# Optimization experiments

Hardware: AMD Instinct MI355X
Metric: run time of the kernel (lower is better)

Reference implementation:

```python
import jax, jax.numpy as jnp
import numpy as np

GROUPS = 32
EPS = 1e-5

def setup_inputs() -> dict:
    key = jax.random.key(0)
    ks = jax.random.split(key, 3)
    b, c, h, w = 4, 256, 64, 64
    x = jax.random.normal(ks[0], (b, c, h, w), dtype=jnp.float32)
    gn_w = jnp.ones((c,), jnp.float32)
    gn_b = jnp.zeros((c,), jnp.float32)
    qkv_w = jax.random.normal(ks[1], (3 * c, c), jnp.float32) * (1.0 / np.sqrt(c))
    qkv_b = jnp.zeros((3 * c,), jnp.float32)
    out_w = jax.random.normal(ks[2], (c, c), jnp.float32) * (1.0 / np.sqrt(c))
    out_b = jnp.zeros((c,), jnp.float32)
    return {"x": x, "gn_w": gn_w, "gn_b": gn_b, "qkv_w": qkv_w,
            "qkv_b": qkv_b, "out_w": out_w, "out_b": out_b}

def reference(x, gn_w, gn_b, qkv_w, qkv_b, out_w, out_b):
    b, c, h, w = x.shape
    scale = c ** (-0.5)
    # GroupNorm over (c/groups, h, w) per group, per-channel affine
    xg = x.reshape(b, GROUPS, c // GROUPS, h, w)
    mean = xg.mean(axis=(2, 3, 4), keepdims=True)
    var = xg.var(axis=(2, 3, 4), keepdims=True)
    xn = ((xg - mean) * jax.lax.rsqrt(var + EPS)).reshape(b, c, h, w)
    xn = xn * gn_w[None, :, None, None] + gn_b[None, :, None, None]
    # 1x1 conv to qkv: [b,3c,h,w]
    qkv = jnp.einsum('bchw,oc->bohw', xn, qkv_w) + qkv_b[None, :, None, None]
    q, k, v = jnp.split(qkv, 3, axis=1)
    # hw_to_seq: [b,c,h,w] -> [b, n, c]
    to_seq = lambda t: t.reshape(b, c, h * w).transpose(0, 2, 1)
    q, k, v = to_seq(q), to_seq(k), to_seq(v)
    sim = jnp.einsum('bic,bjc->bij', q, k) * scale  # [b,n,n]
    attn = jax.nn.softmax(sim, axis=-1)
    out = jnp.einsum('bij,bjc->bic', attn, v)  # [b,n,c]
    out = out.transpose(0, 2, 1).reshape(b, c, h, w)
    out = jnp.einsum('bchw,oc->bohw', out, out_w) + out_b[None, :, None, None]
    return out + x
```

## Files before the change

kernel.cpp:

```cpp
#include <hip/hip_runtime.h>
#include <hip/hip_bf16.h>
#include <stdint.h>

typedef __attribute__((ext_vector_type(8))) short bf16x8;
typedef __attribute__((ext_vector_type(4))) float f32x4;
typedef __attribute__((ext_vector_type(16))) float f32x16;

typedef __attribute__((address_space(1))) const uint32_t gu32;
typedef __attribute__((address_space(3))) uint32_t lu32;

#define N_PIX 4096
#define C_CH  256
#define KVB   128
#define SCALE_LOG2E (0.0625f * 1.4426950408889634f)

__device__ __forceinline__ unsigned short f2bf(float f) {
    unsigned int u = __float_as_uint(f);
    unsigned int r = (u + 0x7FFFu + ((u >> 16) & 1u)) >> 16;
    return (unsigned short)r;
}
__device__ __forceinline__ float bf2f(short s) {
    return __uint_as_float(((unsigned int)(unsigned short)s) << 16);
}

__global__ void prep_kernel(const float* __restrict__ x,
                            const float* __restrict__ gn_w,
                            const float* __restrict__ gn_b,
                            const float* __restrict__ qkv_w,
                            const float* __restrict__ out_w,
                            float* __restrict__ a_out,
                            float* __restrict__ b_out,
                            unsigned short* __restrict__ wq,
                            unsigned short* __restrict__ w2) {
    int bid = blockIdx.x;
    if (bid >= 128) {
        int i = (bid - 128) * 256 + threadIdx.x;
        wq[i] = f2bf(qkv_w[i]);
        if (i < 65536) w2[i] = f2bf(out_w[i]);
        return;
    }
    int b = bid >> 5, g = bid & 31;
    const float* base = x + ((size_t)(b * C_CH + g * 8)) * N_PIX;
    float s1 = 0.f, s2 = 0.f;
    for (int i = threadIdx.x; i < 8 * N_PIX; i += 256) {
        float v = base[i];
        s1 += v; s2 += v * v;
    }
    __shared__ float r1[256], r2[256];
    r1[threadIdx.x] = s1; r2[threadIdx.x] = s2;
    __syncthreads();
    for (int off = 128; off > 0; off >>= 1) {
        if (threadIdx.x < off) {
            r1[threadIdx.x] += r1[threadIdx.x + off];
            r2[threadIdx.x] += r2[threadIdx.x + off];
        }
        __syncthreads();
    }
    if (threadIdx.x < 8) {
        float mean = r1[0] * (1.f / 32768.f);
        float var  = r2[0] * (1.f / 32768.f) - mean * mean;
        float rstd = rsqrtf(var + 1e-5f);
        int c = g * 8 + threadIdx.x;
        float A = rstd * gn_w[c];
        a_out[b * C_CH + c] = A;
        b_out[b * C_CH + c] = gn_b[c] - mean * A;
    }
}

__global__ __launch_bounds__(256)
void qkv_gemm_kernel(const float* __restrict__ x,
                     const float* __restrict__ a_arr,
                     const float* __restrict__ bb_arr,
                     const unsigned short* __restrict__ wq,
                     const float* __restrict__ qkv_b,
                     unsigned short* __restrict__ q_seq,
                     unsigned short* __restrict__ k_seq,
                     unsigned short* __restrict__ vT) {
    __shared__ char wlds[2][16384];
    int pb   = blockIdx.x;
    int och  = blockIdx.y;
    int b    = blockIdx.z;
    int tid  = threadIdx.x;
    int wave = tid >> 6;
    int lane = tid & 63;
    int lo = lane & 15, hi = lane >> 4;
    int prow = pb * 64 + wave * 16 + lo;
    const float* xb = x + (size_t)b * C_CH * N_PIX;
    const float* av = a_arr + b * C_CH;
    const float* bv = bb_arr + b * C_CH;

    auto stageW = [&](int buf, int ks) {
#pragma unroll
        for (int pass = 0; pass < 4; pass++) {
            int chunk = pass * 256 + tid;
            int r = chunk >> 2, cslot = chunk & 3;
            const char* src = (const char*)wq + (size_t)(och * 256 + r) * 512
                              + ks * 64 + cslot * 16;
            __builtin_amdgcn_global_load_lds((gu32*)src,
                                             (lu32*)(wlds[buf] + chunk * 16), 16, 0, 0);
        }
    };

    f32x4 acc[16];
#pragma unroll
    for (int t = 0; t < 16; t++) acc[t] = (f32x4)0.f;

    stageW(0, 0);
    __syncthreads();

#pragma unroll
    for (int ks = 0; ks < 8; ks++) {
        int buf = ks & 1;
        if (ks < 7) stageW(buf ^ 1, ks + 1);
        int c0 = ks * 32 + hi * 8;
        bf16x8 afrag;
#pragma unroll
        for (int i = 0; i < 8; i++) {
            float xv = xb[(size_t)(c0 + i) * N_PIX + prow];
            float v  = fmaf(av[c0 + i], xv, bv[c0 + i]);
            afrag[i] = (short)f2bf(v);
        }
#pragma unroll
        for (int t = 0; t < 16; t++) {
            bf16x8 bfrag = *(const bf16x8*)(wlds[buf] + (t * 16 + lo) * 64 + hi * 16);
            acc[t] = __builtin_amdgcn_mfma_f32_16x16x32_bf16(afrag, bfrag, acc[t], 0, 0, 0);
        }
        __syncthreads();
    }

    int p_base = pb * 64 + wave * 16 + hi * 4;
#pragma unroll
    for (int t = 0; t < 16; t++) {
        int o = och * 256 + t * 16 + lo;
        float bias = qkv_b[o];
        if (och == 2) {
            ushort4 pk;
            pk.x = f2bf(acc[t][0] + bias);
            pk.y = f2bf(acc[t][1] + bias);
            pk.z = f2bf(acc[t][2] + bias);
            pk.w = f2bf(acc[t][3] + bias);
            *(ushort4*)(vT + ((size_t)(b * C_CH + (o - 512))) * N_PIX + p_base) = pk;
        } else {
            float sc = (och == 0) ? SCALE_LOG2E : 1.f;
            unsigned short* dst = (och == 0 ? q_seq : k_seq) + (size_t)b * N_PIX * C_CH;
            int cc = o - och * 256;
#pragma unroll
            for (int r = 0; r < 4; r++)
                dst[(size_t)(p_base + r) * 256 + cc] = f2bf((acc[t][r] + bias) * sc);
        }
    }
}

__global__ __launch_bounds__(512, 2)
void attn_kernel(const unsigned short* __restrict__ q_seq,
                 const unsigned short* __restrict__ k_seq,
                 const unsigned short* __restrict__ vT,
                 unsigned short* __restrict__ o_part,
                 float* __restrict__ m_part,
                 float* __restrict__ l_part) {
    extern __shared__ char lds[];
    char* Kt = lds;
    char* Vt = lds + 65536;
    float* Ml = (float*)(lds + 131072);
    float* Ll = (float*)(lds + 132096);

    int bid  = blockIdx.x;
    int work = (bid & 7) * 32 + (bid >> 3);
    int group = work >> 5;
    int b    = group >> 1;
    int half = group & 1;
    int pq   = work & 31;
    int tid = threadIdx.x;
    int wave = tid >> 6, lane = tid & 63;
    int l31 = lane & 31, hi2 = lane >> 5;
    int qg = wave >> 1, kvh = wave & 1;
    int p0 = pq * 128 + qg * 32;

    const unsigned short* qb = q_seq + (size_t)b * N_PIX * C_CH;
    const unsigned short* kb = k_seq + (size_t)b * N_PIX * C_CH;
    const unsigned short* vb = vT    + (size_t)b * C_CH * N_PIX;

    int ktrow = tid >> 5, kcol = tid & 31;
    int vtrow = tid >> 4, vcol = tid & 15;

    bf16x8 qf[16];
#pragma unroll
    for (int cs = 0; cs < 16; cs++)
        qf[cs] = *(const bf16x8*)(qb + (size_t)(p0 + l31) * 256 + cs * 16 + hi2 * 8);

    f32x16 oacc[8];
#pragma unroll
    for (int t = 0; t < 8; t++) oacc[t] = (f32x16)0.f;
    float m = -1e30f, lsum = 0.f;

    int kswz = l31 << 4;
    int vswz = (l31 & 15) << 4;

    for (int t = 0; t < 16; t++) {
        if (t) __syncthreads();
        int j0 = half * 2048 + t * KVB;
#pragma unroll
        for (int p = 0; p < 8; p++) {
            int kr = p * 16 + ktrow;
            const char* ksrc = (const char*)(kb + (size_t)(j0 + kr) * 256)
                               + ((kcol ^ (kr & 31)) << 4);
            __builtin_amdgcn_global_load_lds((gu32*)ksrc, (lu32*)(Kt + p * 8192 + tid * 16), 16, 0, 0);
            int vr = p * 32 + vtrow;
            const char* vsrc = (const char*)(vb + (size_t)vr * N_PIX + j0)
                               + ((vcol ^ (vr & 15)) << 4);
            __builtin_amdgcn_global_load_lds((gu32*)vsrc, (lu32*)(Vt + p * 8192 + tid * 16), 16, 0, 0);
        }
        __syncthreads();

#pragma unroll
        for (int sub = 0; sub < 2; sub++) {
            int kvb = kvh * 64 + sub * 32;

            f32x16 sacc = (f32x16)0.f;
            __builtin_amdgcn_s_setprio(1);
#pragma unroll
            for (int cs = 0; cs < 16; cs++) {
                bf16x8 kf = *(const bf16x8*)(Kt + (kvb + l31) * 512 + ((cs * 32 + hi2 * 16) ^ kswz));
                sacc = __builtin_amdgcn_mfma_f32_32x32x16_bf16(kf, qf[cs], sacc, 0, 0, 0);
            }
            __builtin_amdgcn_s_setprio(0);

            float mx = sacc[0];
#pragma unroll
            for (int r = 1; r < 16; r++) mx = fmaxf(mx, sacc[r]);
            mx = fmaxf(mx, __shfl_xor(mx, 32, 64));
            if (__any(mx > m + 8.f)) {
                float mC = fmaxf(m, mx);
                float al = __builtin_amdgcn_exp2f(m - mC);
                m = mC; lsum *= al;
#pragma unroll
                for (int r = 0; r < 16; r++) {
                    int qr = (r & 3) + 8 * (r >> 2) + 4 * hi2;
                    float ar = __shfl(al, qr, 64);
#pragma unroll
                    for (int ct = 0; ct < 8; ct++) oacc[ct][r] *= ar;
                }
            }
            f32x16 pexp;
            float psum = 0.f;
#pragma unroll
            for (int r = 0; r < 16; r++) {
                float pe = __builtin_amdgcn_exp2f(sacc[r] - m);
                pexp[r] = pe; psum += pe;
            }
            psum += __shfl_xor(psum, 32, 64);
            lsum += psum;

            bf16x8 pa0, pa1;
            {
                unsigned int x0, x1, y0, y1;
                asm("v_cvt_pk_bf16_f32 %0, %1, %2" : "=v"(x0) : "v"(pexp[0]), "v"(pexp[1]));
                asm("v_cvt_pk_bf16_f32 %0, %1, %2" : "=v"(x1) : "v"(pexp[2]), "v"(pexp[3]));
                asm("v_cvt_pk_bf16_f32 %0, %1, %2" : "=v"(y0) : "v"(pexp[4]), "v"(pexp[5]));
                asm("v_cvt_pk_bf16_f32 %0, %1, %2" : "=v"(y1) : "v"(pexp[6]), "v"(pexp[7]));
                asm("v_permlane32_swap_b32 %0, %1" : "+v"(x0), "+v"(y0));
                asm("v_permlane32_swap_b32 %0, %1" : "+v"(x1), "+v"(y1));
                union { unsigned int u[4]; bf16x8 v; } f0;
                f0.u[0] = x0; f0.u[1] = x1; f0.u[2] = y0; f0.u[3] = y1;
                pa0 = f0.v;
                asm("v_cvt_pk_bf16_f32 %0, %1, %2" : "=v"(x0) : "v"(pexp[8]), "v"(pexp[9]));
                asm("v_cvt_pk_bf16_f32 %0, %1, %2" : "=v"(x1) : "v"(pexp[10]), "v"(pexp[11]));
                asm("v_cvt_pk_bf16_f32 %0, %1, %2" : "=v"(y0) : "v"(pexp[12]), "v"(pexp[13]));
                asm("v_cvt_pk_bf16_f32 %0, %1, %2" : "=v"(y1) : "v"(pexp[14]), "v"(pexp[15]));
                asm("v_permlane32_swap_b32 %0, %1" : "+v"(x0), "+v"(y0));
                asm("v_permlane32_swap_b32 %0, %1" : "+v"(x1), "+v"(y1));
                union { unsigned int u[4]; bf16x8 v; } f1;
                f1.u[0] = x0; f1.u[1] = x1; f1.u[2] = y0; f1.u[3] = y1;
                pa1 = f1.v;
            }

            __builtin_amdgcn_s_setprio(1);
#pragma unroll
            for (int ct = 0; ct < 8; ct++) {
                int c = ct * 32 + l31;
                bf16x8 vf0 = *(const bf16x8*)(Vt + c * 256 + ((kvb * 2 + hi2 * 16) ^ vswz));
                oacc[ct] = __builtin_amdgcn_mfma_f32_32x32x16_bf16(pa0, vf0, oacc[ct], 0, 0, 0);
                bf16x8 vf1 = *(const bf16x8*)(Vt + c * 256 + ((kvb * 2 + 32 + hi2 * 16) ^ vswz));
                oacc[ct] = __builtin_amdgcn_mfma_f32_32x32x16_bf16(pa1, vf1, oacc[ct], 0, 0, 0);
            }
            __builtin_amdgcn_s_setprio(0);
        }
    }
    __syncthreads();

    char* Ow = lds + wave * 16384;
#pragma unroll
    for (int ct = 0; ct < 8; ct++) {
#pragma unroll
        for (int r = 0; r < 16; r++) {
            int q = (r & 3) + 8 * (r >> 2) + 4 * hi2;
            int cb = (ct * 32 + l31) * 2;
            *(unsigned short*)(Ow + q * 512 + (cb ^ (q << 4))) = f2bf(oacc[ct][r]);
        }
    }
    if (lane < 32) { Ml[wave * 32 + lane] = m; Ll[wave * 32 + lane] = lsum; }
    __syncthreads();

    int ql = tid >> 2;
    int qr = ql & 31, qg2 = ql >> 5;
    float g[2];
    float m0 = Ml[(qg2 * 2 + 0) * 32 + qr];
    float m1 = Ml[(qg2 * 2 + 1) * 32 + qr];
    float mm = fmaxf(m0, m1);
    g[0] = __builtin_amdgcn_exp2f(m0 - mm);
    g[1] = __builtin_amdgcn_exp2f(m1 - mm);
    float ls = g[0] * Ll[(qg2 * 2 + 0) * 32 + qr] + g[1] * Ll[(qg2 * 2 + 1) * 32 + qr];
    int qglob = pq * 128 + ql;
    size_t pbase = (size_t)(half * 4 + b) * N_PIX;
    if ((tid & 3) == 0) {
        m_part[pbase + qglob] = mm;
        l_part[pbase + qglob] = ls;
    }
    unsigned short* orow = o_part + (pbase + qglob) * C_CH;
#pragma unroll
    for (int i = 0; i < 8; i++) {
        int s = i * 4 + (tid & 3);
        int cb = (s * 16) ^ (qr << 4);
        bf16x8 a0 = *(const bf16x8*)(lds + (size_t)(qg2 * 2 + 0) * 16384 + qr * 512 + cb);
        bf16x8 a1 = *(const bf16x8*)(lds + (size_t)(qg2 * 2 + 1) * 16384 + qr * 512 + cb);
        union { unsigned short u[8]; bf16x8 v; } pk;
#pragma unroll
        for (int j = 0; j < 8; j++)
            pk.u[j] = f2bf(g[0] * bf2f(a0[j]) + g[1] * bf2f(a1[j]));
        *(bf16x8*)(orow + s * 8) = pk.v;
    }
}

__global__ __launch_bounds__(256)
void combine_kernel(const unsigned short* __restrict__ o_part,
                    const float* __restrict__ m_part,
                    const float* __restrict__ l_part,
                    const unsigned short* __restrict__ w2,
                    const float* __restrict__ out_b,
                    const float* __restrict__ x,
                    float* __restrict__ y) {
    int bid = blockIdx.x;
    int b = bid >> 7, pr = bid & 127;
    int tid = threadIdx.x;
    int wave = tid >> 6, lane = tid & 63;
    int lo = lane & 15, hi = lane >> 4;
    int rowgrp = wave & 1, ohalf = wave >> 1;
    int p0 = pr * 32 + rowgrp * 16;
    int row = p0 + lo;
    size_t i0 = (size_t)b * N_PIX + row;
    size_t i1 = (size_t)(4 + b) * N_PIX + row;
    float m0 = m_part[i0], l0 = l_part[i0];
    float m1 = m_part[i1], l1 = l_part[i1];
    float mm = fmaxf(m0, m1);
    float e0 = __builtin_amdgcn_exp2f(m0 - mm), e1 = __builtin_amdgcn_exp2f(m1 - mm);
    float rl = 1.f / (l0 * e0 + l1 * e1);
    float f0 = e0 * rl, f1 = e1 * rl;
    const unsigned short* P0 = o_part + i0 * C_CH;
    const unsigned short* P1 = o_part + i1 * C_CH;

    f32x4 acc2[8];
#pragma unroll
    for (int t = 0; t < 8; t++) acc2[t] = (f32x4)0.f;

#pragma unroll
    for (int ks = 0; ks < 8; ks++) {
        int c0 = ks * 32 + hi * 8;
        bf16x8 a0 = *(const bf16x8*)(P0 + c0);
        bf16x8 a1 = *(const bf16x8*)(P1 + c0);
        bf16x8 of;
#pragma unroll
        for (int i = 0; i < 8; i++)
            of[i] = (short)f2bf(bf2f(a0[i]) * f0 + bf2f(a1[i]) * f1);
#pragma unroll
        for (int ot = 0; ot < 8; ot++) {
            int o = ohalf * 128 + ot * 16 + lo;
            bf16x8 wf = *(const bf16x8*)(w2 + (size_t)o * 256 + c0);
            acc2[ot] = __builtin_amdgcn_mfma_f32_16x16x32_bf16(of, wf, acc2[ot], 0, 0, 0);
        }
    }

    int p_base = p0 + hi * 4;
#pragma unroll
    for (int ot = 0; ot < 8; ot++) {
        int o = ohalf * 128 + ot * 16 + lo;
        float bias = out_b[o];
        size_t off = ((size_t)(b * C_CH + o)) * N_PIX + p_base;
        f32x4 xv = *(const f32x4*)(x + off);
        f32x4 outv;
#pragma unroll
        for (int r = 0; r < 4; r++) outv[r] = acc2[ot][r] + bias + xv[r];
        *(f32x4*)(y + off) = outv;
    }
}

extern "C" void kernel_launch(void* const* d_in, const int* in_sizes, int n_in,
                              void* d_out, int out_size, void* d_ws, size_t ws_size,
                              hipStream_t stream) {
    const float* x     = (const float*)d_in[0];
    const float* gn_w  = (const float*)d_in[1];
    const float* gn_b  = (const float*)d_in[2];
    const float* qkv_w = (const float*)d_in[3];
    const float* qkv_b = (const float*)d_in[4];
    const float* out_w = (const float*)d_in[5];
    const float* out_b = (const float*)d_in[6];
    float* y = (float*)d_out;
    char* ws = (char*)d_ws;

    float* a_arr  = (float*)(ws);
    float* bb_arr = (float*)(ws + 4096);
    unsigned short* wq     = (unsigned short*)(ws + 8192);
    unsigned short* w2     = (unsigned short*)(ws + 401408);
    unsigned short* q_seq  = (unsigned short*)(ws + 532480);
    unsigned short* k_seq  = (unsigned short*)(ws + 532480 + 8388608);
    unsigned short* vT     = (unsigned short*)(ws + 532480 + 2 * 8388608);
    unsigned short* o_part = (unsigned short*)(ws + 532480 + 3 * 8388608);
    float* m_part = (float*)(ws + 42475520);
    float* l_part = (float*)(ws + 42606592);

    (void)hipFuncSetAttribute((const void*)attn_kernel,
                              hipFuncAttributeMaxDynamicSharedMemorySize, 133120);

    prep_kernel<<<896, 256, 0, stream>>>(x, gn_w, gn_b, qkv_w, out_w,
                                         a_arr, bb_arr, wq, w2);
    qkv_gemm_kernel<<<dim3(64, 3, 4), 256, 0, stream>>>(x, a_arr, bb_arr, wq, qkv_b,
                                                        q_seq, k_seq, vT);
    attn_kernel<<<256, 512, 133120, stream>>>(q_seq, k_seq, vT, o_part, m_part, l_part);
    combine_kernel<<<512, 256, 0, stream>>>(o_part, m_part, l_part, w2, out_b, x, y);
}
```

Baseline: 173.2 us.

## Stage normalized activation tile in LDS once and loop over q/k/v outputs

The QKV GEMM now normalizes and converts a 64-pixel by 256-channel activation tile to bf16 once per block into a swizzled LDS buffer. It reuses that tile for all three output groups (q, k, v) instead of launching a separate block per group that each re-read x from global memory. This cuts redundant global reads and GroupNorm math by a factor of three. The cost is a third as many blocks (256 instead of 768), more dynamic LDS per block, and a longer serial loop per block, which may reduce parallelism.

```diff
diff --git a/kernel.cpp b/kernel.cpp
--- a/kernel.cpp
+++ b/kernel.cpp
@@ -76,20 +76,39 @@
                      unsigned short* __restrict__ q_seq,
                      unsigned short* __restrict__ k_seq,
                      unsigned short* __restrict__ vT) {
-    __shared__ char wlds[2][16384];
-    int pb   = blockIdx.x;
-    int och  = blockIdx.y;
-    int b    = blockIdx.z;
-    int tid  = threadIdx.x;
-    int wave = tid >> 6;
-    int lane = tid & 63;
+    extern __shared__ char qlds[];
+    char* Ab = qlds;
+    char* wlds0 = qlds + 32768;
+    char* wlds1 = qlds + 49152;
+    int pb = blockIdx.x;
+    int b  = blockIdx.y;
+    int tid = threadIdx.x;
+    int wave = tid >> 6, lane = tid & 63;
     int lo = lane & 15, hi = lane >> 4;
-    int prow = pb * 64 + wave * 16 + lo;
     const float* xb = x + (size_t)b * C_CH * N_PIX;
     const float* av = a_arr + b * C_CH;
     const float* bv = bb_arr + b * C_CH;
 
-    auto stageW = [&](int buf, int ks) {
+    {
+        int px = lane;
+        int cblk = wave;
+        int gpx = pb * 64 + px;
+#pragma unroll
+        for (int i = 0; i < 8; i++) {
+            int c0 = cblk * 64 + i * 8;
+            union { unsigned short u[8]; bf16x8 v; } pk;
+#pragma unroll
+            for (int j = 0; j < 8; j++) {
+                float xv = xb[(size_t)(c0 + j) * N_PIX + gpx];
+                pk.u[j] = f2bf(fmaf(av[c0 + j], xv, bv[c0 + j]));
+            }
+            int slot = ((c0 >> 3) ^ (px & 31));
+            *(bf16x8*)(Ab + px * 512 + slot * 16) = pk.v;
+        }
+    }
+
+    auto stageW = [&](char* dst, int w) {
+        int och = w >> 3, ks = w & 7;
 #pragma unroll
         for (int pass = 0; pass < 4; pass++) {
             int chunk = pass * 256 + tid;
@@ -97,56 +116,53 @@
             const char* src = (const char*)wq + (size_t)(och * 256 + r) * 512
                               + ks * 64 + cslot * 16;
             __builtin_amdgcn_global_load_lds((gu32*)src,
-                                             (lu32*)(wlds[buf] + chunk * 16), 16, 0, 0);
+                                             (lu32*)(dst + chunk * 16), 16, 0, 0);
         }
     };
 
-    f32x4 acc[16];
-#pragma unroll
-    for (int t = 0; t < 16; t++) acc[t] = (f32x4)0.f;
-
-    stageW(0, 0);
+    stageW(wlds0, 0);
     __syncthreads();
 
-#pragma unroll
-    for (int ks = 0; ks < 8; ks++) {
-        int buf = ks & 1;
-        if (ks < 7) stageW(buf ^ 1, ks + 1);
-        int c0 = ks * 32 + hi * 8;
-        bf16x8 afrag;
-#pragma unroll
-        for (int i = 0; i < 8; i++) {
-            float xv = xb[(size_t)(c0 + i) * N_PIX + prow];
-            float v  = fmaf(av[c0 + i], xv, bv[c0 + i]);
-            afrag[i] = (short)f2bf(v);
+    int p_base = pb * 64 + wave * 16 + hi * 4;
+    int arow = wave * 16 + lo;
+    for (int och = 0; och < 3; och++) {
+        f32x4 acc[16];
+#pragma unroll
+        for (int t = 0; t < 16; t++) acc[t] = (f32x4)0.f;
+#pragma unroll
+        for (int ks = 0; ks < 8; ks++) {
+            int w = och * 8 + ks;
+            char* cur = (w & 1) ? wlds1 : wlds0;
+            char* nxt = (w & 1) ? wlds0 : wlds1;
+            if (w < 23) stageW(nxt, w + 1);
+            int slot = (ks * 4 + hi) ^ (arow & 31);
+            bf16x8 afrag = *(const bf16x8*)(Ab + arow * 512 + slot * 16);
+#pragma unroll
+            for (int t = 0; t < 16; t++) {
+                bf16x8 bfrag = *(const bf16x8*)(cur + (t * 16 + lo) * 64 + hi * 16);
+                acc[t] = __builtin_amdgcn_mfma_f32_16x16x32_bf16(afrag, bfrag, acc[t], 0, 0, 0);
+            }
+            __syncthreads();
         }
 #pragma unroll
         for (int t = 0; t < 16; t++) {
-            bf16x8 bfrag = *(const bf16x8*)(wlds[buf] + (t * 16 + lo) * 64 + hi * 16);
-            acc[t] = __builtin_amdgcn_mfma_f32_16x16x32_bf16(afrag, bfrag, acc[t], 0, 0, 0);
-        }
-        __syncthreads();
-    }
-
-    int p_base = pb * 64 + wave * 16 + hi * 4;
-#pragma unroll
-    for (int t = 0; t < 16; t++) {
-        int o = och * 256 + t * 16 + lo;
-        float bias = qkv_b[o];
-        if (och == 2) {
-            ushort4 pk;
-            pk.x = f2bf(acc[t][0] + bias);
-            pk.y = f2bf(acc[t][1] + bias);
-            pk.z = f2bf(acc[t][2] + bias);
-            pk.w = f2bf(acc[t][3] + bias);
-            *(ushort4*)(vT + ((size_t)(b * C_CH + (o - 512))) * N_PIX + p_base) = pk;
-        } else {
-            float sc = (och == 0) ? SCALE_LOG2E : 1.f;
-            unsigned short* dst = (och == 0 ? q_seq : k_seq) + (size_t)b * N_PIX * C_CH;
-            int cc = o - och * 256;
-#pragma unroll
-            for (int r = 0; r < 4; r++)
-                dst[(size_t)(p_base + r) * 256 + cc] = f2bf((acc[t][r] + bias) * sc);
+            int o = och * 256 + t * 16 + lo;
+            float bias = qkv_b[o];
+            if (och == 2) {
+                ushort4 pk;
+                pk.x = f2bf(acc[t][0] + bias);
+                pk.y = f2bf(acc[t][1] + bias);
+                pk.z = f2bf(acc[t][2] + bias);
+                pk.w = f2bf(acc[t][3] + bias);
+                *(ushort4*)(vT + ((size_t)(b * C_CH + (o - 512))) * N_PIX + p_base) = pk;
+            } else {
+                float sc = (och == 0) ? SCALE_LOG2E : 1.f;
+                unsigned short* dst = (och == 0 ? q_seq : k_seq) + (size_t)b * N_PIX * C_CH;
+                int cc = o - och * 256;
+#pragma unroll
+                for (int r = 0; r < 4; r++)
+                    dst[(size_t)(p_base + r) * 256 + cc] = f2bf((acc[t][r] + bias) * sc);
+            }
         }
     }
 }
@@ -419,11 +435,13 @@
 
     (void)hipFuncSetAttribute((const void*)attn_kernel,
                               hipFuncAttributeMaxDynamicSharedMemorySize, 133120);
+    (void)hipFuncSetAttribute((const void*)qkv_gemm_kernel,
+                              hipFuncAttributeMaxDynamicSharedMemorySize, 65536);
 
     prep_kernel<<<896, 256, 0, stream>>>(x, gn_w, gn_b, qkv_w, out_w,
                                          a_arr, bb_arr, wq, w2);
-    qkv_gemm_kernel<<<dim3(64, 3, 4), 256, 0, stream>>>(x, a_arr, bb_arr, wq, qkv_b,
-                                                        q_seq, k_seq, vT);
+    qkv_gemm_kernel<<<dim3(64, 4), 256, 65536, stream>>>(x, a_arr, bb_arr, wq, qkv_b,
+                                                         q_seq, k_seq, vT);
     attn_kernel<<<256, 512, 133120, stream>>>(q_seq, k_seq, vT, o_part, m_part, l_part);
     combine_kernel<<<512, 256, 0, stream>>>(o_part, m_part, l_part, w2, out_b, x, y);
 }
```

Result: slower. 184.8 us (+6.7%).

## Shrink attention blocks to 64 queries and 64-key tiles with new V layout

Applied to the files above, without the earlier changes.

The attention kernel now runs 256-thread blocks covering 64 queries each, with 64-key KV tiles, doubling the grid to 512 blocks and halving the LDS footprint. The V tile gets a new swizzled layout that packs two channels per LDS row. The aim is to let two independent blocks share a CU so one block's loads overlap the other's compute. In exchange, K/V data is reused across fewer queries, so global traffic doubles, and there are twice as many barriers per key processed.

```diff
diff --git a/kernel.cpp b/kernel.cpp
--- a/kernel.cpp
+++ b/kernel.cpp
@@ -11,7 +11,6 @@
 
 #define N_PIX 4096
 #define C_CH  256
-#define KVB   128
 #define SCALE_LOG2E (0.0625f * 1.4426950408889634f)
 
 __device__ __forceinline__ unsigned short f2bf(float f) {
@@ -151,7 +150,7 @@
     }
 }
 
-__global__ __launch_bounds__(512, 2)
+__global__ __launch_bounds__(256, 2)
 void attn_kernel(const unsigned short* __restrict__ q_seq,
                  const unsigned short* __restrict__ k_seq,
                  const unsigned short* __restrict__ vT,
@@ -160,29 +159,27 @@
                  float* __restrict__ l_part) {
     extern __shared__ char lds[];
     char* Kt = lds;
-    char* Vt = lds + 65536;
-    float* Ml = (float*)(lds + 131072);
-    float* Ll = (float*)(lds + 132096);
+    char* Vt = lds + 32768;
+    float* Ml = (float*)(lds + 65536);
+    float* Ll = (float*)(lds + 66048);
 
     int bid  = blockIdx.x;
-    int work = (bid & 7) * 32 + (bid >> 3);
-    int group = work >> 5;
+    int work = (bid & 7) * 64 + (bid >> 3);
+    int group = work >> 6;
     int b    = group >> 1;
     int half = group & 1;
-    int pq   = work & 31;
+    int pq   = work & 63;
     int tid = threadIdx.x;
     int wave = tid >> 6, lane = tid & 63;
     int l31 = lane & 31, hi2 = lane >> 5;
     int qg = wave >> 1, kvh = wave & 1;
-    int p0 = pq * 128 + qg * 32;
+    int p0 = pq * 64 + qg * 32;
+    int kvb = kvh * 32;
 
     const unsigned short* qb = q_seq + (size_t)b * N_PIX * C_CH;
     const unsigned short* kb = k_seq + (size_t)b * N_PIX * C_CH;
     const unsigned short* vb = vT    + (size_t)b * C_CH * N_PIX;
 
-    int ktrow = tid >> 5, kcol = tid & 31;
-    int vtrow = tid >> 4, vcol = tid & 15;
-
     bf16x8 qf[16];
 #pragma unroll
     for (int cs = 0; cs < 16; cs++)
@@ -194,97 +191,101 @@
     float m = -1e30f, lsum = 0.f;
 
     int kswz = l31 << 4;
-    int vswz = (l31 & 15) << 4;
-
-    for (int t = 0; t < 16; t++) {
+
+    for (int t = 0; t < 32; t++) {
         if (t) __syncthreads();
-        int j0 = half * 2048 + t * KVB;
+        int j0 = half * 2048 + t * 64;
+        const char* vjb = (const char*)vb + (size_t)j0 * 2;
 #pragma unroll
         for (int p = 0; p < 8; p++) {
-            int kr = p * 16 + ktrow;
+            int kr = p * 8 + (tid >> 5);
+            int ks = tid & 31;
             const char* ksrc = (const char*)(kb + (size_t)(j0 + kr) * 256)
-                               + ((kcol ^ (kr & 31)) << 4);
-            __builtin_amdgcn_global_load_lds((gu32*)ksrc, (lu32*)(Kt + p * 8192 + tid * 16), 16, 0, 0);
-            int vr = p * 32 + vtrow;
-            const char* vsrc = (const char*)(vb + (size_t)vr * N_PIX + j0)
-                               + ((vcol ^ (vr & 15)) << 4);
-            __builtin_amdgcn_global_load_lds((gu32*)vsrc, (lu32*)(Vt + p * 8192 + tid * 16), 16, 0, 0);
+                               + ((ks ^ (kr & 31)) << 4);
+            __builtin_amdgcn_global_load_lds((gu32*)ksrc,
+                                             (lu32*)(Kt + p * 4096 + tid * 16), 16, 0, 0);
+            int vr = p * 16 + (tid >> 4);
+            int vs = tid & 15;
+            int tt = vs ^ (vr & 15);
+            int c  = 2 * vr + (tt >> 3);
+            __builtin_amdgcn_global_load_lds(
+                (gu32*)(vjb + (size_t)c * 8192 + ((tt & 7) << 4)),
+                (lu32*)(Vt + p * 4096 + tid * 16), 16, 0, 0);
         }
         __syncthreads();
 
-#pragma unroll
-        for (int sub = 0; sub < 2; sub++) {
-            int kvb = kvh * 64 + sub * 32;
-
-            f32x16 sacc = (f32x16)0.f;
-            __builtin_amdgcn_s_setprio(1);
-#pragma unroll
-            for (int cs = 0; cs < 16; cs++) {
-                bf16x8 kf = *(const bf16x8*)(Kt + (kvb + l31) * 512 + ((cs * 32 + hi2 * 16) ^ kswz));
-                sacc = __builtin_amdgcn_mfma_f32_32x32x16_bf16(kf, qf[cs], sacc, 0, 0, 0);
+        f32x16 sacc = (f32x16)0.f;
+        __builtin_amdgcn_s_setprio(1);
+#pragma unroll
+        for (int cs = 0; cs < 16; cs++) {
+            bf16x8 kf = *(const bf16x8*)(Kt + (kvb + l31) * 512 + ((cs * 32 + hi2 * 16) ^ kswz));
+            sacc = __builtin_amdgcn_mfma_f32_32x32x16_bf16(kf, qf[cs], sacc, 0, 0, 0);
+        }
+        __builtin_amdgcn_s_setprio(0);
+
+        float mx = sacc[0];
+#pragma unroll
+        for (int r = 1; r < 16; r++) mx = fmaxf(mx, sacc[r]);
+        mx = fmaxf(mx, __shfl_xor(mx, 32, 64));
+        if (__any(mx > m + 8.f)) {
+            float mC = fmaxf(m, mx);
+            float al = __builtin_amdgcn_exp2f(m - mC);
+            m = mC; lsum *= al;
+#pragma unroll
+            for (int r = 0; r < 16; r++) {
+                int qr = (r & 3) + 8 * (r >> 2) + 4 * hi2;
+                float ar = __shfl(al, qr, 64);
+#pragma unroll
+                for (int ct = 0; ct < 8; ct++) oacc[ct][r] *= ar;
             }
-            __builtin_amdgcn_s_setprio(0);
-
-            float mx = sacc[0];
-#pragma unroll
-            for (int r = 1; r < 16; r++) mx = fmaxf(mx, sacc[r]);
-            mx = fmaxf(mx, __shfl_xor(mx, 32, 64));
-            if (__any(mx > m + 8.f)) {
-                float mC = fmaxf(m, mx);
-                float al = __builtin_amdgcn_exp2f(m - mC);
-                m = mC; lsum *= al;
-#pragma unroll
-                for (int r = 0; r < 16; r++) {
-                    int qr = (r & 3) + 8 * (r >> 2) + 4 * hi2;
-                    float ar = __shfl(al, qr, 64);
-#pragma unroll
-                    for (int ct = 0; ct < 8; ct++) oacc[ct][r] *= ar;
-                }
-            }
-            f32x16 pexp;
-            float psum = 0.f;
-#pragma unroll
-            for (int r = 0; r < 16; r++) {
-                float pe = __builtin_amdgcn_exp2f(sacc[r] - m);
-                pexp[r] = pe; psum += pe;
-            }
-            psum += __shfl_xor(psum, 32, 64);
-            lsum += psum;
-
-            bf16x8 pa0, pa1;
-            {
-                unsigned int x0, x1, y0, y1;
-                asm("v_cvt_pk_bf16_f32 %0, %1, %2" : "=v"(x0) : "v"(pexp[0]), "v"(pexp[1]));
-                asm("v_cvt_pk_bf16_f32 %0, %1, %2" : "=v"(x1) : "v"(pexp[2]), "v"(pexp[3]));
-                asm("v_cvt_pk_bf16_f32 %0, %1, %2" : "=v"(y0) : "v"(pexp[4]), "v"(pexp[5]));
-                asm("v_cvt_pk_bf16_f32 %0, %1, %2" : "=v"(y1) : "v"(pexp[6]), "v"(pexp[7]));
-                asm("v_permlane32_swap_b32 %0, %1" : "+v"(x0), "+v"(y0));
-                asm("v_permlane32_swap_b32 %0, %1" : "+v"(x1), "+v"(y1));
-                union { unsigned int u[4]; bf16x8 v; } f0;
-                f0.u[0] = x0; f0.u[1] = x1; f0.u[2] = y0; f0.u[3] = y1;
-                pa0 = f0.v;
-                asm("v_cvt_pk_bf16_f32 %0, %1, %2" : "=v"(x0) : "v"(pexp[8]), "v"(pexp[9]));
-                asm("v_cvt_pk_bf16_f32 %0, %1, %2" : "=v"(x1) : "v"(pexp[10]), "v"(pexp[11]));
-                asm("v_cvt_pk_bf16_f32 %0, %1, %2" : "=v"(y0) : "v"(pexp[12]), "v"(pexp[13]));
-                asm("v_cvt_pk_bf16_f32 %0, %1, %2" : "=v"(y1) : "v"(pexp[14]), "v"(pexp[15]));
-                asm("v_permlane32_swap_b32 %0, %1" : "+v"(x0), "+v"(y0));
-                asm("v_permlane32_swap_b32 %0, %1" : "+v"(x1), "+v"(y1));
-                union { unsigned int u[4]; bf16x8 v; } f1;
-                f1.u[0] = x0; f1.u[1] = x1; f1.u[2] = y0; f1.u[3] = y1;
-                pa1 = f1.v;
-            }
-
-            __builtin_amdgcn_s_setprio(1);
-#pragma unroll
-            for (int ct = 0; ct < 8; ct++) {
-                int c = ct * 32 + l31;
-                bf16x8 vf0 = *(const bf16x8*)(Vt + c * 256 + ((kvb * 2 + hi2 * 16) ^ vswz));
-                oacc[ct] = __builtin_amdgcn_mfma_f32_32x32x16_bf16(pa0, vf0, oacc[ct], 0, 0, 0);
-                bf16x8 vf1 = *(const bf16x8*)(Vt + c * 256 + ((kvb * 2 + 32 + hi2 * 16) ^ vswz));
-                oacc[ct] = __builtin_amdgcn_mfma_f32_32x32x16_bf16(pa1, vf1, oacc[ct], 0, 0, 0);
-            }
-            __builtin_amdgcn_s_setprio(0);
-        }
+        }
+        f32x16 pexp;
+        float psum = 0.f;
+#pragma unroll
+        for (int r = 0; r < 16; r++) {
+            float pe = __builtin_amdgcn_exp2f(sacc[r] - m);
+            pexp[r] = pe; psum += pe;
+        }
+        psum += __shfl_xor(psum, 32, 64);
+        lsum += psum;
+
+        bf16x8 pa0, pa1;
+        {
+            unsigned int x0, x1, y0, y1;
+            asm("v_cvt_pk_bf16_f32 %0, %1, %2" : "=v"(x0) : "v"(pexp[0]), "v"(pexp[1]));
+            asm("v_cvt_pk_bf16_f32 %0, %1, %2" : "=v"(x1) : "v"(pexp[2]), "v"(pexp[3]));
+            asm("v_cvt_pk_bf16_f32 %0, %1, %2" : "=v"(y0) : "v"(pexp[4]), "v"(pexp[5]));
+            asm("v_cvt_pk_bf16_f32 %0, %1, %2" : "=v"(y1) : "v"(pexp[6]), "v"(pexp[7]));
+            asm("v_permlane32_swap_b32 %0, %1" : "+v"(x0), "+v"(y0));
+            asm("v_permlane32_swap_b32 %0, %1" : "+v"(x1), "+v"(y1));
+            union { unsigned int u[4]; bf16x8 v; } f0;
+            f0.u[0] = x0; f0.u[1] = x1; f0.u[2] = y0; f0.u[3] = y1;
+            pa0 = f0.v;
+            asm("v_cvt_pk_bf16_f32 %0, %1, %2" : "=v"(x0) : "v"(pexp[8]), "v"(pexp[9]));
+            asm("v_cvt_pk_bf16_f32 %0, %1, %2" : "=v"(x1) : "v"(pexp[10]), "v"(pexp[11]));
+            asm("v_cvt_pk_bf16_f32 %0, %1, %2" : "=v"(y0) : "v"(pexp[12]), "v"(pexp[13]));
+            asm("v_cvt_pk_bf16_f32 %0, %1, %2" : "=v"(y1) : "v"(pexp[14]), "v"(pexp[15]));
+            asm("v_permlane32_swap_b32 %0, %1" : "+v"(x0), "+v"(y0));
+            asm("v_permlane32_swap_b32 %0, %1" : "+v"(x1), "+v"(y1));
+            union { unsigned int u[4]; bf16x8 v; } f1;
+            f1.u[0] = x0; f1.u[1] = x1; f1.u[2] = y0; f1.u[3] = y1;
+            pa1 = f1.v;
+        }
+
+        __builtin_amdgcn_s_setprio(1);
+#pragma unroll
+        for (int ct = 0; ct < 8; ct++) {
+            int c = ct * 32 + l31;
+            int vrow = c >> 1;
+            int sb = (c & 1) * 8;
+            int s0i = sb + kvh * 4 + hi2;
+            bf16x8 vf0 = *(const bf16x8*)(Vt + vrow * 256 + ((s0i ^ (vrow & 15)) << 4));
+            oacc[ct] = __builtin_amdgcn_mfma_f32_32x32x16_bf16(pa0, vf0, oacc[ct], 0, 0, 0);
+            int s1i = s0i + 2;
+            bf16x8 vf1 = *(const bf16x8*)(Vt + vrow * 256 + ((s1i ^ (vrow & 15)) << 4));
+            oacc[ct] = __builtin_amdgcn_mfma_f32_32x32x16_bf16(pa1, vf1, oacc[ct], 0, 0, 0);
+        }
+        __builtin_amdgcn_s_setprio(0);
     }
     __syncthreads();
 
@@ -310,7 +311,7 @@
     g[0] = __builtin_amdgcn_exp2f(m0 - mm);
     g[1] = __builtin_amdgcn_exp2f(m1 - mm);
     float ls = g[0] * Ll[(qg2 * 2 + 0) * 32 + qr] + g[1] * Ll[(qg2 * 2 + 1) * 32 + qr];
-    int qglob = pq * 128 + ql;
+    int qglob = pq * 64 + ql;
     size_t pbase = (size_t)(half * 4 + b) * N_PIX;
     if ((tid & 3) == 0) {
         m_part[pbase + qglob] = mm;
@@ -418,12 +419,12 @@
     float* l_part = (float*)(ws + 42606592);
 
     (void)hipFuncSetAttribute((const void*)attn_kernel,
-                              hipFuncAttributeMaxDynamicSharedMemorySize, 133120);
+                              hipFuncAttributeMaxDynamicSharedMemorySize, 66560);
 
     prep_kernel<<<896, 256, 0, stream>>>(x, gn_w, gn_b, qkv_w, out_w,
                                          a_arr, bb_arr, wq, w2);
     qkv_gemm_kernel<<<dim3(64, 3, 4), 256, 0, stream>>>(x, a_arr, bb_arr, wq, qkv_b,
                                                         q_seq, k_seq, vT);
-    attn_kernel<<<256, 512, 133120, stream>>>(q_seq, k_seq, vT, o_part, m_part, l_part);
+    attn_kernel<<<512, 256, 66560, stream>>>(q_seq, k_seq, vT, o_part, m_part, l_part);
     combine_kernel<<<512, 256, 0, stream>>>(o_part, m_part, l_part, w2, out_b, x, y);
 }
```

Result: slower. 181.4 us (+4.7%).
